# Kernel tuning notes

Hardware: AMD Instinct MI355X
Metric: run time of the kernel (lower is better)

The kernel has to match this reference:

```python
import jax, jax.numpy as jnp
import numpy as np

B, C, CI, H, W = 8, 64, 32, 48, 48
BN_EPS = 1e-5


def setup_inputs() -> dict:
    key = jax.random.key(0)
    ks = jax.random.split(key, 13)
    s = lambda k, shape: jax.random.normal(k, shape, dtype=jnp.float32)
    return {
        "x": s(ks[0], (B, C, H, W)),
        "g_w": s(ks[1], (CI, C)) * 0.1,
        "g_b": s(ks[2], (CI,)) * 0.1,
        "th_w": s(ks[3], (CI, C)) * 0.1,
        "th_b": s(ks[4], (CI,)) * 0.1,
        "ph_w": s(ks[5], (CI, C)) * 0.1,
        "ph_b": s(ks[6], (CI,)) * 0.1,
        "cp_wt": s(ks[7], (CI,)) * 0.1,
        "cp_wp": s(ks[8], (CI,)) * 0.1,
        "W_w": s(ks[9], (C, CI)) * 0.1,
        "W_b": s(ks[10], (C,)) * 0.1,
        "bn_g": s(ks[11], (C,)),
        "bn_b": s(ks[12], (C,)),
    }


def reference(x, g_w, g_b, th_w, th_b, ph_w, ph_b, cp_wt, cp_wp, W_w, W_b, bn_g, bn_b):
    b, c, h, w = x.shape
    n = h * w
    xf = x.reshape(b, c, n)  # flatten spatial
    # 1x1 convs == per-position matmuls over channels -> (b, n, ci)
    g_x = jnp.einsum("ic,bcn->bni", g_w, xf) + g_b
    theta = jnp.einsum("ic,bcn->bni", th_w, xf) + th_b
    phi = jnp.einsum("ic,bcn->bni", ph_w, xf) + ph_b
    # concat_project(concat(theta_i, phi_j)) = relu(wt.theta_i + wp.phi_j)
    a = theta @ cp_wt  # (b, n) -- theta-row scores
    bscore = phi @ cp_wp  # (b, n) -- phi-col scores
    f_div = jax.nn.relu(a[:, :, None] + bscore[:, None, :]) * (1.0 / n)  # (b,n,n)
    y = jnp.einsum("bnm,bmi->bni", f_div, g_x)  # (b, n, ci)
    # W: 1x1 conv back to C, then BatchNorm2d (training-mode batch stats)
    wy = jnp.einsum("ci,bni->bcn", W_w, y) + W_b[None, :, None]  # (b, c, n)
    mean = wy.mean(axis=(0, 2), keepdims=True)
    var = wy.var(axis=(0, 2), keepdims=True)
    wy = (wy - mean) * jax.lax.rsqrt(var + BN_EPS)
    wy = wy * bn_g[None, :, None] + bn_b[None, :, None]
    return wy.reshape(b, c, h, w) + x
```

## Files before the change

### kernel.cpp

```cpp
#include <hip/hip_runtime.h>
#include <math.h>

#define B 8
#define C 64
#define CI 32
#define N 2304
#define NT 36
#define NTILES (B*NT)
#define NTOT (B*N)
#define BN_EPS 1e-5

#define OFF_GX   0
#define OFF_A    (OFF_GX + B*N*CI)
#define OFF_C    (OFF_A + B*N)
#define OFF_SC   (OFF_C + B*N)
#define OFF_SIDX (OFF_SC + B*N)
#define OFF_KN   (OFF_SIDX + B*N)
#define OFF_PLOC (OFF_KN + B*N)
#define OFF_TOT  (OFF_PLOC + B*N*64)
#define OFF_PART (OFF_TOT + B*NT*64)
#define OFF_WY   (OFF_PART + NTILES*128)

__global__ __launch_bounds__(256) void k_proj(
    const float* __restrict__ x,
    const float* __restrict__ g_w, const float* __restrict__ g_b,
    const float* __restrict__ th_w, const float* __restrict__ th_b,
    const float* __restrict__ ph_w, const float* __restrict__ ph_b,
    const float* __restrict__ cp_wt, const float* __restrict__ cp_wp,
    float* __restrict__ ws)
{
    __shared__ float gw[CI*C];
    __shared__ float tw[C], pw[C];
    __shared__ float gb[CI];
    __shared__ float tpb[2];
    const int tid = threadIdx.x;
    const int blk = blockIdx.x;
    const int b  = blk / NT;
    const int n0 = (blk % NT) * 64;

    for (int i = tid; i < CI*C; i += 256) gw[i] = g_w[i];
    if (tid < C) {
        float s = 0.f;
        for (int i = 0; i < CI; i++) s += cp_wt[i] * th_w[i*C + tid];
        tw[tid] = s;
    } else if (tid < 2*C) {
        int c = tid - C; float s = 0.f;
        for (int i = 0; i < CI; i++) s += cp_wp[i] * ph_w[i*C + c];
        pw[c] = s;
    } else if (tid < 2*C + CI) {
        gb[tid - 2*C] = g_b[tid - 2*C];
    } else if (tid == 2*C + CI) {
        float s = 0.f; for (int i = 0; i < CI; i++) s += cp_wt[i]*th_b[i]; tpb[0] = s;
    } else if (tid == 2*C + CI + 1) {
        float s = 0.f; for (int i = 0; i < CI; i++) s += cp_wp[i]*ph_b[i]; tpb[1] = s;
    }
    __syncthreads();

    const int p = tid & 63, wv = tid >> 6;
    const int n = n0 + p;
    const int ch0 = wv*8;
    const float* xb = x + (size_t)b*C*N + n;
    float accg[8];
    #pragma unroll
    for (int j = 0; j < 8; j++) accg[j] = 0.f;
    float aa = 0.f, cc = 0.f;
    #pragma unroll 4
    for (int c4 = 0; c4 < C; c4 += 4) {
        float xv0 = xb[(size_t)(c4+0)*N];
        float xv1 = xb[(size_t)(c4+1)*N];
        float xv2 = xb[(size_t)(c4+2)*N];
        float xv3 = xb[(size_t)(c4+3)*N];
        if (wv == 0) {
            float4 t4 = *(const float4*)(tw + c4);
            aa += t4.x*xv0 + t4.y*xv1 + t4.z*xv2 + t4.w*xv3;
        } else if (wv == 1) {
            float4 p4 = *(const float4*)(pw + c4);
            cc += p4.x*xv0 + p4.y*xv1 + p4.z*xv2 + p4.w*xv3;
        }
        #pragma unroll
        for (int j = 0; j < 8; j++) {
            float4 g4 = *(const float4*)(gw + (ch0+j)*C + c4);
            accg[j] += g4.x*xv0 + g4.y*xv1 + g4.z*xv2 + g4.w*xv3;
        }
    }
    #pragma unroll
    for (int j = 0; j < 8; j++) accg[j] += gb[ch0 + j];
    float* gxp = ws + OFF_GX + ((size_t)(b*N + n))*CI + ch0;
    *(float4*)(gxp)     = make_float4(accg[0], accg[1], accg[2], accg[3]);
    *(float4*)(gxp + 4) = make_float4(accg[4], accg[5], accg[6], accg[7]);
    if (wv == 0) ws[OFF_A + b*N + n] = aa + tpb[0];
    else if (wv == 1) ws[OFF_C + b*N + n] = cc + tpb[1];
}

__global__ __launch_bounds__(256) void k_rank(float* __restrict__ ws)
{
    __shared__ __align__(16) unsigned long long keys[N];
    __shared__ int partial[256];
    __shared__ int partial2[256];
    __shared__ float av[64];
    const int tid = threadIdx.x;
    const int blk = blockIdx.x;
    const int b  = blk / NT;
    const int m0 = (blk % NT) * 64;
    const float* cb = ws + OFF_C + (size_t)b*N;
    for (int i = tid; i < N; i += 256) {
        unsigned int u = __float_as_uint(cb[i]);
        unsigned int k32 = (u & 0x80000000u) ? ~u : (u | 0x80000000u);
        keys[i] = ((unsigned long long)k32 << 12) | (unsigned long long)(4095 - i);
    }
    if (tid < 64) av[tid] = ws[OFF_A + b*N + m0 + tid];
    __syncthreads();
    const int p = tid & 63;
    const int wv = tid >> 6;
    const unsigned long long my = keys[m0 + p];
    unsigned int ua  = __float_as_uint(-av[p]);
    unsigned int t32 = (ua & 0x80000000u) ? ~ua : (ua | 0x80000000u);
    const unsigned long long thr = ((unsigned long long)t32 << 12) | 4095ull;
    const ulonglong2* kp = (const ulonglong2*)keys;
    int c0=0,c1=0,c2=0,c3=0, d0=0,d1=0,d2=0,d3=0;
    const int base = wv * (N/8);
    #pragma unroll 4
    for (int t2 = 0; t2 < N/8; t2 += 2) {
        ulonglong2 ka = kp[base + t2];
        ulonglong2 kb = kp[base + t2 + 1];
        c0 += (ka.x > my);  c1 += (ka.y > my);
        c2 += (kb.x > my);  c3 += (kb.y > my);
        d0 += (ka.x > thr); d1 += (ka.y > thr);
        d2 += (kb.x > thr); d3 += (kb.y > thr);
    }
    partial[tid]  = (c0 + c1) + (c2 + c3);
    partial2[tid] = (d0 + d1) + (d2 + d3);
    __syncthreads();
    if (tid < 64) {
        int rank = partial[tid] + partial[tid+64] + partial[tid+128] + partial[tid+192];
        int kc   = partial2[tid] + partial2[tid+64] + partial2[tid+128] + partial2[tid+192];
        unsigned long long km = keys[m0 + tid];
        unsigned int k32 = (unsigned int)(km >> 12);
        unsigned int u = (k32 & 0x80000000u) ? (k32 & 0x7fffffffu) : ~k32;
        ws[OFF_SC + b*N + rank] = __uint_as_float(u);
        ((int*)(ws + OFF_SIDX))[b*N + rank] = m0 + tid;
        ((int*)(ws + OFF_KN))[b*N + m0 + tid] = kc;
    }
}

__global__ __launch_bounds__(256) void k_prefix(float* __restrict__ ws)
{
    __shared__ int   sidx[64];
    __shared__ float scv[64];
    __shared__ float pl_lds[64*64];
    __shared__ float wtot[4*64];
    __shared__ float segoff[4*64];
    const int tid = threadIdx.x;
    const int blk = blockIdx.x;
    const int b = blk / NT, t = blk % NT;
    const int k0 = t * 64;
    if (tid < 64) {
        sidx[tid] = ((const int*)(ws + OFF_SIDX))[b*N + k0 + tid];
        scv[tid]  = ws[OFF_SC + b*N + k0 + tid];
    }
    __syncthreads();
    const int w   = tid >> 6;
    const int ch  = tid & 63;
    const int chm = ch & 31;
    const bool isCG = ch >= 32;
    const float* gx = ws + OFF_GX + (size_t)b*N*CI;
    float acc = 0.f;
    #pragma unroll
    for (int kk = 0; kk < 16; kk++) {
        int k = w*16 + kk;
        int m = sidx[k];
        float gval = gx[(size_t)m*CI + chm];
        float v = isCG ? gval * scv[k] : gval;
        pl_lds[k*64 + ch] = acc;
        acc += v;
    }
    wtot[w*64 + ch] = acc;
    __syncthreads();
    if (tid < 64) {
        float s = 0.f;
        #pragma unroll
        for (int ww = 0; ww < 4; ww++) { segoff[ww*64 + tid] = s; s += wtot[ww*64 + tid]; }
        ws[OFF_TOT + ((size_t)b*NT + t)*64 + tid] = s;
    }
    __syncthreads();
    float* pl = ws + OFF_PLOC + ((size_t)b*N + k0)*64;
    #pragma unroll
    for (int r4 = 0; r4 < 16; r4++) {
        int r = (tid >> 6) + r4*4;
        pl[(size_t)r*64 + ch] = pl_lds[r*64 + ch] + segoff[(r >> 4)*64 + ch];
    }
}

__global__ __launch_bounds__(256) void k_stats(
    const float* __restrict__ W_w, const float* __restrict__ W_b,
    float* __restrict__ ws)
{
    __shared__ float offs_lds[(NT+1)*64];
    __shared__ float y_lds[64*33];
    __shared__ float Wl[C*CI];
    __shared__ float Wbl[C];
    const int tid = threadIdx.x;
    const int blk = blockIdx.x;
    const int b = blk / NT, tile = blk % NT;

    for (int i = tid; i < C*CI; i += 256) Wl[i] = W_w[i];
    if (tid < C) Wbl[tid] = W_b[tid];
    {
        const float* tot = ws + OFF_TOT + (size_t)b*NT*64;
        for (int i = tid; i < NT*64; i += 256) offs_lds[i] = tot[i];
    }
    __syncthreads();
    if (tid < 64) {
        float acc = 0.f;
        #pragma unroll 4
        for (int t = 0; t < NT; t++) {
            float v = offs_lds[t*64 + tid];
            offs_lds[t*64 + tid] = acc;
            acc += v;
        }
        offs_lds[NT*64 + tid] = acc;
    }
    __syncthreads();

    const int p = tid & 63, wv = tid >> 6;
    const int n = tile*64 + p;
    const float an = ws[OFF_A + b*N + n];
    const int k = ((const int*)(ws + OFF_KN))[b*N + n];
    const int kt = k >> 6;
    const float* pl = ws + OFF_PLOC + ((size_t)b*N + k)*64;
    const float inv_n = 1.0f / (float)N;
    #pragma unroll
    for (int q = 0; q < 8; q++) {
        int i = wv*8 + q;
        float plg = (k < N) ? pl[i]      : 0.f;
        float plc = (k < N) ? pl[i + 32] : 0.f;
        float Pg = offs_lds[kt*64 + i]      + plg;
        float Pc = offs_lds[kt*64 + i + 32] + plc;
        y_lds[p*33 + i] = inv_n * (an * Pg + Pc);
    }
    __syncthreads();

    float yv[CI];
    #pragma unroll
    for (int i = 0; i < CI; i++) yv[i] = y_lds[p*33 + i];

    const int lane = tid & 63;
    float* part = ws + OFF_PART + (size_t)blk*128;
    float* wyb  = ws + OFF_WY + (size_t)b*C*N + n;
    #pragma unroll
    for (int q = 0; q < 16; q++) {
        int c = wv*16 + q;
        float wyv = Wbl[c];
        #pragma unroll
        for (int i4 = 0; i4 < CI; i4 += 4) {
            float4 w4 = *(const float4*)(Wl + c*CI + i4);
            wyv += w4.x*yv[i4] + w4.y*yv[i4+1] + w4.z*yv[i4+2] + w4.w*yv[i4+3];
        }
        wyb[(size_t)c*N] = wyv;
        float s = wyv, sq = wyv * wyv;
        #pragma unroll
        for (int off = 32; off >= 1; off >>= 1) {
            s  += __shfl_xor(s,  off, 64);
            sq += __shfl_xor(sq, off, 64);
        }
        if (lane == 0) { part[c] = s; part[64 + c] = sq; }
    }
}

__global__ __launch_bounds__(256) void k_final(
    const float* __restrict__ x,
    const float* __restrict__ bn_g, const float* __restrict__ bn_b,
    const float* __restrict__ ws, float* __restrict__ out)
{
    __shared__ double red[256];
    __shared__ float ssc[128];
    const int tid = threadIdx.x;
    {
        const float* part = ws + OFF_PART;
        const int ch = tid & 127, half = tid >> 7;
        double acc = 0.0;
        #pragma unroll 8
        for (int k2 = 0; k2 < NTILES/2; k2++)
            acc += (double)part[(size_t)(half*(NTILES/2) + k2)*128 + ch];
        red[tid] = acc;
    }
    __syncthreads();
    if (tid < 64) {
        double ssum = red[tid]      + red[tid + 128];
        double ssq  = red[tid + 64] + red[tid + 192];
        double mean = ssum / (double)NTOT;
        double var  = ssq / (double)NTOT - mean*mean;
        float rs  = (float)(1.0 / sqrt(var + BN_EPS));
        float scl = bn_g[tid] * rs;
        ssc[tid]      = scl;
        ssc[64 + tid] = bn_b[tid] - (float)mean * scl;
    }
    __syncthreads();
    const float4* wy4 = (const float4*)(ws + OFF_WY);
    const float4* x4p = (const float4*)x;
    float4*       o4p = (float4*)out;
    #pragma unroll
    for (int j = 0; j < 4; j++) {
        const int idx = blockIdx.x*1024 + j*256 + tid;
        const float4 w4 = wy4[idx];
        const float4 xv = x4p[idx];
        const int c = ((idx*4) / N) & 63;
        const float s = ssc[c], sh = ssc[64 + c];
        float4 o;
        o.x = w4.x*s + sh + xv.x;
        o.y = w4.y*s + sh + xv.y;
        o.z = w4.z*s + sh + xv.z;
        o.w = w4.w*s + sh + xv.w;
        o4p[idx] = o;
    }
}

extern "C" void kernel_launch(void* const* d_in, const int* in_sizes, int n_in,
                              void* d_out, int out_size, void* d_ws, size_t ws_size,
                              hipStream_t stream)
{
    const float* x     = (const float*)d_in[0];
    const float* g_w   = (const float*)d_in[1];
    const float* g_b   = (const float*)d_in[2];
    const float* th_w  = (const float*)d_in[3];
    const float* th_b  = (const float*)d_in[4];
    const float* ph_w  = (const float*)d_in[5];
    const float* ph_b  = (const float*)d_in[6];
    const float* cp_wt = (const float*)d_in[7];
    const float* cp_wp = (const float*)d_in[8];
    const float* W_w   = (const float*)d_in[9];
    const float* W_b   = (const float*)d_in[10];
    const float* bn_g  = (const float*)d_in[11];
    const float* bn_b  = (const float*)d_in[12];
    float* ws  = (float*)d_ws;
    float* out = (float*)d_out;

    hipLaunchKernelGGL(k_proj,   dim3(NTILES), dim3(256), 0, stream,
                       x, g_w, g_b, th_w, th_b, ph_w, ph_b, cp_wt, cp_wp, ws);
    hipLaunchKernelGGL(k_rank,   dim3(NTILES), dim3(256), 0, stream, ws);
    hipLaunchKernelGGL(k_prefix, dim3(NTILES), dim3(256), 0, stream, ws);
    hipLaunchKernelGGL(k_stats,  dim3(NTILES), dim3(256), 0, stream, W_w, W_b, ws);
    hipLaunchKernelGGL(k_final,  dim3(NTILES), dim3(256), 0, stream,
                       x, bn_g, bn_b, ws, out);
}
```

Before: 64.04 us.

## Fuse projection and ranking; replace O(N^2) rank count with bucketed counting sort

Merges the projection and rank kernels into one launch. Each block recomputes the phi-scores for its whole batch row and builds a 2048-bucket histogram of the top key bits in shared memory. It then does a prefix scan and scatters the keys into bucket order. Ranks and threshold counts are found by scanning only the matching bucket instead of comparing against all N keys. This removes one launch and the quadratic compare loop, at the cost of each block redundantly computing scores for all 2304 positions and heavy shared-memory and atomic use.

```diff
diff --git a/kernel.cpp b/kernel.cpp
--- a/kernel.cpp
+++ b/kernel.cpp
@@ -12,16 +12,15 @@
 
 #define OFF_GX   0
 #define OFF_A    (OFF_GX + B*N*CI)
-#define OFF_C    (OFF_A + B*N)
-#define OFF_SC   (OFF_C + B*N)
+#define OFF_SC   (OFF_A + B*N)
 #define OFF_SIDX (OFF_SC + B*N)
 #define OFF_KN   (OFF_SIDX + B*N)
 #define OFF_PLOC (OFF_KN + B*N)
 #define OFF_TOT  (OFF_PLOC + B*N*64)
-#define OFF_PART (OFF_TOT + B*NT*64)
+#define OFF_PART (OFF_TOT + NTILES*64)
 #define OFF_WY   (OFF_PART + NTILES*128)
 
-__global__ __launch_bounds__(256) void k_proj(
+__global__ __launch_bounds__(256) void k_projrank(
     const float* __restrict__ x,
     const float* __restrict__ g_w, const float* __restrict__ g_b,
     const float* __restrict__ th_w, const float* __restrict__ th_b,
@@ -29,14 +28,25 @@
     const float* __restrict__ cp_wt, const float* __restrict__ cp_wp,
     float* __restrict__ ws)
 {
+    __shared__ unsigned long long su64[N];
     __shared__ float gw[CI*C];
     __shared__ float tw[C], pw[C];
     __shared__ float gb[CI];
     __shared__ float tpb[2];
+    __shared__ float av[64];
+    __shared__ unsigned int mkey[64];
+    __shared__ unsigned int hist[2048];
+    __shared__ unsigned int cursor[2048];
+    __shared__ unsigned int offs[2049];
+    __shared__ int partial[256];
+    __shared__ int wavetot[4];
+
     const int tid = threadIdx.x;
     const int blk = blockIdx.x;
-    const int b  = blk / NT;
+    const int b = blk / NT;
     const int n0 = (blk % NT) * 64;
+    const int tile6 = n0 >> 6;
+    const int p = tid & 63, wv = tid >> 6;
 
     for (int i = tid; i < CI*C; i += 256) gw[i] = g_w[i];
     if (tid < C) {
@@ -54,92 +64,126 @@
     } else if (tid == 2*C + CI + 1) {
         float s = 0.f; for (int i = 0; i < CI; i++) s += cp_wp[i]*ph_b[i]; tpb[1] = s;
     }
-    __syncthreads();
-
-    const int p = tid & 63, wv = tid >> 6;
-    const int n = n0 + p;
-    const int ch0 = wv*8;
-    const float* xb = x + (size_t)b*C*N + n;
-    float accg[8];
-    #pragma unroll
-    for (int j = 0; j < 8; j++) accg[j] = 0.f;
-    float aa = 0.f, cc = 0.f;
-    #pragma unroll 4
-    for (int c4 = 0; c4 < C; c4 += 4) {
-        float xv0 = xb[(size_t)(c4+0)*N];
-        float xv1 = xb[(size_t)(c4+1)*N];
-        float xv2 = xb[(size_t)(c4+2)*N];
-        float xv3 = xb[(size_t)(c4+3)*N];
-        if (wv == 0) {
+    #pragma unroll
+    for (int i = tid; i < 2048; i += 256) hist[i] = 0u;
+    __syncthreads();
+
+    unsigned int k32r[9];
+    #pragma unroll
+    for (int r = 0; r < 9; r++) {
+        const int j = tid + (r << 8);
+        const float* xj = x + (size_t)b*C*N + j;
+        float aa = 0.f, cc = 0.f;
+        #pragma unroll 4
+        for (int c4 = 0; c4 < C; c4 += 4) {
+            float xv0 = xj[(size_t)(c4+0)*N];
+            float xv1 = xj[(size_t)(c4+1)*N];
+            float xv2 = xj[(size_t)(c4+2)*N];
+            float xv3 = xj[(size_t)(c4+3)*N];
             float4 t4 = *(const float4*)(tw + c4);
+            float4 p4 = *(const float4*)(pw + c4);
             aa += t4.x*xv0 + t4.y*xv1 + t4.z*xv2 + t4.w*xv3;
-        } else if (wv == 1) {
-            float4 p4 = *(const float4*)(pw + c4);
             cc += p4.x*xv0 + p4.y*xv1 + p4.z*xv2 + p4.w*xv3;
         }
-        #pragma unroll
-        for (int j = 0; j < 8; j++) {
-            float4 g4 = *(const float4*)(gw + (ch0+j)*C + c4);
-            accg[j] += g4.x*xv0 + g4.y*xv1 + g4.z*xv2 + g4.w*xv3;
-        }
-    }
-    #pragma unroll
-    for (int j = 0; j < 8; j++) accg[j] += gb[ch0 + j];
-    float* gxp = ws + OFF_GX + ((size_t)(b*N + n))*CI + ch0;
-    *(float4*)(gxp)     = make_float4(accg[0], accg[1], accg[2], accg[3]);
-    *(float4*)(gxp + 4) = make_float4(accg[4], accg[5], accg[6], accg[7]);
-    if (wv == 0) ws[OFF_A + b*N + n] = aa + tpb[0];
-    else if (wv == 1) ws[OFF_C + b*N + n] = cc + tpb[1];
-}
-
-__global__ __launch_bounds__(256) void k_rank(float* __restrict__ ws)
-{
-    __shared__ __align__(16) unsigned long long keys[N];
-    __shared__ int partial[256];
-    __shared__ int partial2[256];
-    __shared__ float av[64];
-    const int tid = threadIdx.x;
-    const int blk = blockIdx.x;
-    const int b  = blk / NT;
-    const int m0 = (blk % NT) * 64;
-    const float* cb = ws + OFF_C + (size_t)b*N;
-    for (int i = tid; i < N; i += 256) {
-        unsigned int u = __float_as_uint(cb[i]);
+        aa += tpb[0]; cc += tpb[1];
+        unsigned int u = __float_as_uint(cc);
         unsigned int k32 = (u & 0x80000000u) ? ~u : (u | 0x80000000u);
-        keys[i] = ((unsigned long long)k32 << 12) | (unsigned long long)(4095 - i);
-    }
-    if (tid < 64) av[tid] = ws[OFF_A + b*N + m0 + tid];
-    __syncthreads();
-    const int p = tid & 63;
-    const int wv = tid >> 6;
-    const unsigned long long my = keys[m0 + p];
-    unsigned int ua  = __float_as_uint(-av[p]);
-    unsigned int t32 = (ua & 0x80000000u) ? ~ua : (ua | 0x80000000u);
-    const unsigned long long thr = ((unsigned long long)t32 << 12) | 4095ull;
-    const ulonglong2* kp = (const ulonglong2*)keys;
-    int c0=0,c1=0,c2=0,c3=0, d0=0,d1=0,d2=0,d3=0;
-    const int base = wv * (N/8);
-    #pragma unroll 4
-    for (int t2 = 0; t2 < N/8; t2 += 2) {
-        ulonglong2 ka = kp[base + t2];
-        ulonglong2 kb = kp[base + t2 + 1];
-        c0 += (ka.x > my);  c1 += (ka.y > my);
-        c2 += (kb.x > my);  c3 += (kb.y > my);
-        d0 += (ka.x > thr); d1 += (ka.y > thr);
-        d2 += (kb.x > thr); d3 += (kb.y > thr);
-    }
-    partial[tid]  = (c0 + c1) + (c2 + c3);
-    partial2[tid] = (d0 + d1) + (d2 + d3);
-    __syncthreads();
-    if (tid < 64) {
-        int rank = partial[tid] + partial[tid+64] + partial[tid+128] + partial[tid+192];
-        int kc   = partial2[tid] + partial2[tid+64] + partial2[tid+128] + partial2[tid+192];
-        unsigned long long km = keys[m0 + tid];
-        unsigned int k32 = (unsigned int)(km >> 12);
-        unsigned int u = (k32 & 0x80000000u) ? (k32 & 0x7fffffffu) : ~k32;
-        ws[OFF_SC + b*N + rank] = __uint_as_float(u);
-        ((int*)(ws + OFF_SIDX))[b*N + rank] = m0 + tid;
-        ((int*)(ws + OFF_KN))[b*N + m0 + tid] = kc;
+        k32r[r] = k32;
+        atomicAdd(&hist[2047 - (k32 >> 21)], 1u);
+        if ((j >> 6) == tile6) {
+            av[j & 63] = aa;
+            mkey[j & 63] = k32;
+            ws[OFF_A + (size_t)b*N + j] = aa;
+        }
+    }
+    __syncthreads();
+
+    {
+        const int base8 = tid * 8;
+        int loc[8]; int ssum = 0;
+        #pragma unroll
+        for (int k = 0; k < 8; k++) { loc[k] = ssum; ssum += (int)hist[base8 + k]; }
+        partial[tid] = ssum;
+        __syncthreads();
+        int v = partial[tid];
+        #pragma unroll
+        for (int off = 1; off < 64; off <<= 1) {
+            int u = __shfl_up(v, off, 64);
+            if ((tid & 63) >= off) v += u;
+        }
+        if ((tid & 63) == 63) wavetot[tid >> 6] = v;
+        __syncthreads();
+        int wbase = 0;
+        for (int w = 0; w < (tid >> 6); w++) wbase += wavetot[w];
+        const int excl = wbase + v - partial[tid];
+        #pragma unroll
+        for (int k = 0; k < 8; k++) {
+            unsigned o = (unsigned)(excl + loc[k]);
+            offs[base8 + k] = o;
+            cursor[base8 + k] = o;
+        }
+        if (tid == 0) offs[2048] = N;
+        __syncthreads();
+    }
+
+    #pragma unroll
+    for (int r = 0; r < 9; r++) {
+        const int j = tid + (r << 8);
+        const unsigned int k32 = k32r[r];
+        const unsigned pos = atomicAdd(&cursor[2047 - (k32 >> 21)], 1u);
+        su64[pos] = ((unsigned long long)k32 << 12) | (unsigned long long)(4095 - j);
+    }
+    __syncthreads();
+
+    {
+        const int n = n0 + p;
+        const int ch0 = wv*8;
+        const float* xb = x + (size_t)b*C*N + n;
+        float accg[8];
+        #pragma unroll
+        for (int j = 0; j < 8; j++) accg[j] = 0.f;
+        #pragma unroll 4
+        for (int c4 = 0; c4 < C; c4 += 4) {
+            float xv0 = xb[(size_t)(c4+0)*N];
+            float xv1 = xb[(size_t)(c4+1)*N];
+            float xv2 = xb[(size_t)(c4+2)*N];
+            float xv3 = xb[(size_t)(c4+3)*N];
+            #pragma unroll
+            for (int j = 0; j < 8; j++) {
+                float4 g4 = *(const float4*)(gw + (ch0+j)*C + c4);
+                accg[j] += g4.x*xv0 + g4.y*xv1 + g4.z*xv2 + g4.w*xv3;
+            }
+        }
+        #pragma unroll
+        for (int j = 0; j < 8; j++) accg[j] += gb[ch0 + j];
+        float* gxp = ws + OFF_GX + ((size_t)(b*N + n))*CI + ch0;
+        *(float4*)(gxp)     = make_float4(accg[0], accg[1], accg[2], accg[3]);
+        *(float4*)(gxp + 4) = make_float4(accg[4], accg[5], accg[6], accg[7]);
+    }
+
+    if (tid < 64) {
+        const int m = n0 + tid;
+        const unsigned int k32m = mkey[tid];
+        const unsigned long long my =
+            ((unsigned long long)k32m << 12) | (unsigned long long)(4095 - m);
+        const int bt = 2047 - (int)(k32m >> 21);
+        const int lo = (int)offs[bt], hi = (int)offs[bt + 1];
+        int r = lo;
+        for (int e = lo; e < hi; e++) r += (su64[e] > my) ? 1 : 0;
+        unsigned int u = (k32m & 0x80000000u) ? (k32m & 0x7fffffffu) : ~k32m;
+        ws[OFF_SC + (size_t)b*N + r] = __uint_as_float(u);
+        ((int*)(ws + OFF_SIDX))[(size_t)b*N + r] = m;
+    } else if (tid < 128) {
+        const int p2 = tid - 64;
+        const int n = n0 + p2;
+        unsigned int ua  = __float_as_uint(-av[p2]);
+        unsigned int t32 = (ua & 0x80000000u) ? ~ua : (ua | 0x80000000u);
+        const unsigned long long thr = ((unsigned long long)t32 << 12) | 4095ull;
+        const int bt = 2047 - (int)(t32 >> 21);
+        const int lo = (int)offs[bt], hi = (int)offs[bt + 1];
+        int k = lo;
+        for (int e = lo; e < hi; e++) k += (su64[e] > thr) ? 1 : 0;
+        ((int*)(ws + OFF_KN))[(size_t)b*N + n] = k;
     }
 }
 
@@ -335,11 +379,10 @@
     float* ws  = (float*)d_ws;
     float* out = (float*)d_out;
 
-    hipLaunchKernelGGL(k_proj,   dim3(NTILES), dim3(256), 0, stream,
+    hipLaunchKernelGGL(k_projrank, dim3(NTILES), dim3(256), 0, stream,
                        x, g_w, g_b, th_w, th_b, ph_w, ph_b, cp_wt, cp_wp, ws);
-    hipLaunchKernelGGL(k_rank,   dim3(NTILES), dim3(256), 0, stream, ws);
-    hipLaunchKernelGGL(k_prefix, dim3(NTILES), dim3(256), 0, stream, ws);
-    hipLaunchKernelGGL(k_stats,  dim3(NTILES), dim3(256), 0, stream, W_w, W_b, ws);
-    hipLaunchKernelGGL(k_final,  dim3(NTILES), dim3(256), 0, stream,
+    hipLaunchKernelGGL(k_prefix,   dim3(NTILES), dim3(256), 0, stream, ws);
+    hipLaunchKernelGGL(k_stats,    dim3(NTILES), dim3(256), 0, stream, W_w, W_b, ws);
+    hipLaunchKernelGGL(k_final,    dim3(NTILES), dim3(256), 0, stream,
                        x, bn_g, bn_b, ws, out);
 }
```

Result: slower. 78.04 us (+21.9%).
